# Optimization experiments

Hardware: AMD Instinct MI355X
Metric: run time of the kernel (lower is better)

## Reference

```python
import jax, jax.numpy as jnp
import numpy as np

N_NODES, SEQ, FEAT, HID, NLAYERS = 126, 24, 17, 100, 2


def setup_inputs() -> dict:
    key = jax.random.key(0)
    ks = jax.random.split(key, 14)
    B = 64
    s = 1.0 / np.sqrt(HID)  # torch LSTM default init scale
    inp = {
        "x": jax.random.normal(ks[0], (B, SEQ, N_NODES, FEAT), dtype=jnp.float32),
        # per-node stacked LSTM weights, gate order (i, f, g, o) as in torch
        "W_ih0": jax.random.uniform(ks[1], (N_NODES, 4 * HID, FEAT), jnp.float32, -s, s),
        "W_hh0": jax.random.uniform(ks[2], (N_NODES, 4 * HID, HID), jnp.float32, -s, s),
        "b_ih0": jax.random.uniform(ks[3], (N_NODES, 4 * HID), jnp.float32, -s, s),
        "b_hh0": jax.random.uniform(ks[4], (N_NODES, 4 * HID), jnp.float32, -s, s),
        "W_ih1": jax.random.uniform(ks[5], (N_NODES, 4 * HID, HID), jnp.float32, -s, s),
        "W_hh1": jax.random.uniform(ks[6], (N_NODES, 4 * HID, HID), jnp.float32, -s, s),
        "b_ih1": jax.random.uniform(ks[7], (N_NODES, 4 * HID), jnp.float32, -s, s),
        "b_hh1": jax.random.uniform(ks[8], (N_NODES, 4 * HID), jnp.float32, -s, s),
        "w_lin": jax.random.uniform(ks[9], (1, HID), jnp.float32, -s, s),
        "b_lin": jax.random.uniform(ks[10], (1,), jnp.float32, -s, s),
        "w_end": jax.random.uniform(ks[11], (1, SEQ), jnp.float32, -0.2, 0.2),  # Conv2d(seqlen->1, k=1)
        "b_end": jax.random.uniform(ks[12], (1,), jnp.float32, -0.2, 0.2),
    }
    return inp


def _lstm_cell(xin, h, c, Wih, Whh, bih, bhh):
    # xin: [N,B,Fin], h/c: [N,B,H], Wih: [N,4H,Fin], Whh: [N,4H,H]
    g = (jnp.einsum("nbf,ngf->nbg", xin, Wih)
         + jnp.einsum("nbh,ngh->nbg", h, Whh)
         + (bih + bhh)[:, None, :])
    i, f, gg, o = jnp.split(g, 4, axis=-1)
    c_new = jax.nn.sigmoid(f) * c + jax.nn.sigmoid(i) * jnp.tanh(gg)
    h_new = jax.nn.sigmoid(o) * jnp.tanh(c_new)
    return h_new, c_new


def reference(x, W_ih0, W_hh0, b_ih0, b_hh0, W_ih1, W_hh1, b_ih1, b_hh1,
              w_lin, b_lin, w_end, b_end):
    B, T, N, F = x.shape
    H = W_hh0.shape[-1]
    xt = jnp.transpose(x, (1, 2, 0, 3))  # [T, N, B, F]
    z = jnp.zeros((N, B, H), dtype=x.dtype)

    def step(carry, x_t):
        h1, c1, h2, c2 = carry
        h1, c1 = _lstm_cell(x_t, h1, c1, W_ih0, W_hh0, b_ih0, b_hh0)
        h2, c2 = _lstm_cell(h1, h2, c2, W_ih1, W_hh1, b_ih1, b_hh1)
        return (h1, c1, h2, c2), h2

    (h1, c1, h2, c2), outs = jax.lax.scan(step, (z, z, z, z), xt)  # outs: [T,N,B,H]
    lin = jnp.einsum("tnbh,oh->tnbo", outs, w_lin) + b_lin  # [T,N,B,1]
    lstmlayer = jnp.transpose(lin, (2, 0, 1, 3))  # [B,T,N,1] (matches torch permute(2,1,0,3))
    # Conv2d(seqlen -> out_channels=1, kernel 1x1) over the T channel axis
    out = jnp.einsum("btnj,ct->bcnj", lstmlayer, w_end) + b_end[None, :, None, None]  # [B,1,N,1]
    hn = jnp.stack([h1, h2], axis=1)  # [N, num_layers=2, B, H]
    cn = jnp.stack([c1, c2], axis=1)
    return (out, hn, cn)
```

## Files before the change

kernel.cpp:

```cpp
#include <hip/hip_runtime.h>
#include <hip/hip_bf16.h>

#define NN 126
#define TT 24
#define FF 17
#define HH 100
#define NMT 25

#define AL_SH 51200
#define X0_SH AL_SH
#define X1_SH (AL_SH + 8192)
#define X0BUF 4096
#define X1BUF 7168
#define TOT_SH (X1_SH + 2 * X1BUF)
#define LDS_BYTES (TOT_SH * 2)

typedef __attribute__((ext_vector_type(8))) short short8v;
typedef __attribute__((ext_vector_type(4))) float float4v;

__device__ __forceinline__ short f2bf(float f) {
    union { float f; unsigned u; } v; v.f = f;
    unsigned r = v.u + 0x7FFFu + ((v.u >> 16) & 1u);
    return (short)(r >> 16);
}
#define LOG2E 1.4426950408889634f
__device__ __forceinline__ float sigm_(float x) {
    return __builtin_amdgcn_rcpf(1.0f + __builtin_amdgcn_exp2f(-LOG2E * x));
}
__device__ __forceinline__ float tanh_(float x) {
    return 1.0f - 2.0f * __builtin_amdgcn_rcpf(1.0f + __builtin_amdgcn_exp2f((2.0f * LOG2E) * x));
}

__global__ __launch_bounds__(1024, 4)
void lstm_one(const float* __restrict__ x,
              const float* __restrict__ Wih0, const float* __restrict__ Whh0,
              const float* __restrict__ bih0, const float* __restrict__ bhh0,
              const float* __restrict__ Wih1, const float* __restrict__ Whh1,
              const float* __restrict__ bih1, const float* __restrict__ bhh1,
              const float* __restrict__ wlin, const float* __restrict__ blin,
              const float* __restrict__ wend, const float* __restrict__ bend,
              float* __restrict__ out)
{
    extern __shared__ short lds_s[];
    short* Al = lds_s;
    short* X0 = lds_s + X0_SH;
    short* X1 = lds_s + X1_SH;
    float* red = (float*)lds_s;

    const int n   = blockIdx.x >> 1;
    const int bh  = blockIdx.x & 1;
    const int tid = threadIdx.x, lane = tid & 63, w = tid >> 6;
    const int cl  = lane & 15, q = lane >> 4;
    const int mt0 = (w <= 8) ? (w * 2) : (18 + (w - 9));
    const int nmt = (w <= 8) ? 2 : 1;

    {
        const short8v zz = {0,0,0,0,0,0,0,0};
        for (int i = tid; i < TOT_SH / 8; i += 1024)
            *(short8v*)(lds_s + (size_t)i * 8) = zz;
    }
    __syncthreads();

    {
        const float* W = Whh0 + (size_t)n * 40000;
        for (int i = tid; i < 40000; i += 1024) {
            const int orl = i / 100, j = i - orl * 100;
            const int g = orl / 100, cell = orl - g * 100;
            const int gr = cell * 4 + g;
            const int k = 18 + j;
            Al[(((k >> 5) * NMT + (gr >> 4)) * 64 + ((((k >> 3) & 3) << 4) | (gr & 15))) * 8 + (k & 7)]
                = f2bf(W[i]);
        }
    }
    {
        const float* W = Wih0 + (size_t)n * 6800;
        for (int i = tid; i < 6800; i += 1024) {
            const int orl = i / 17, k = i - orl * 17;
            const int g = orl / 100, cell = orl - g * 100;
            const int gr = cell * 4 + g;
            Al[((gr >> 4) * 64 + ((((k >> 3) & 3) << 4) | (gr & 15))) * 8 + (k & 7)] = f2bf(W[i]);
        }
    }
    if (tid < 400) {
        const int g = tid / 100, cell = tid - g * 100;
        const int gr = cell * 4 + g;
        const int orow = n * 400 + tid;
        Al[((gr >> 4) * 64 + ((2 << 4) | (gr & 15))) * 8 + 1] = f2bf(bih0[orow] + bhh0[orow]);
    }

    short8v wreg[2][7];
    #pragma unroll
    for (int mi = 0; mi < 2; ++mi) {
        if (mi < nmt) {
            const int gr = (mt0 + mi) * 16 + cl;
            const int cell = gr >> 2, g = gr & 3;
            const int orow = n * 400 + g * HH + cell;
            const float* Wi = Wih1 + (size_t)orow * HH;
            const float* Wh = Whh1 + (size_t)orow * HH;
            #pragma unroll
            for (int kt = 0; kt < 7; ++kt) {
                const int k0 = kt * 32 + q * 8;
                float v[8];
                #pragma unroll
                for (int e = 0; e < 8; ++e) v[e] = 0.0f;
                if (k0 == 0) {
                    v[0] = bih1[orow] + bhh1[orow];
                    v[4] = Wi[0]; v[5] = Wi[1]; v[6] = Wi[2]; v[7] = Wi[3];
                } else if (k0 <= 96) {
                    #pragma unroll
                    for (int e = 0; e < 8; ++e) v[e] = Wi[k0 - 4 + e];
                } else if (k0 >= 104 && k0 <= 192) {
                    #pragma unroll
                    for (int e = 0; e < 8; ++e) v[e] = Wh[k0 - 104 + e];
                } else if (k0 == 200) {
                    v[0] = Wh[96]; v[1] = Wh[97]; v[2] = Wh[98]; v[3] = Wh[99];
                }
                short8v pv;
                #pragma unroll
                for (int e = 0; e < 8; ++e) pv[e] = f2bf(v[e]);
                wreg[mi][kt] = pv;
            }
        }
    }

    int aX0h1[2][2], aX1h1[2][2], aX1h2[2][2];
    #pragma unroll
    for (int mi = 0; mi < 2; ++mi) {
        const int cell = (mt0 + mi) * 4 + q;
        #pragma unroll
        for (int nh = 0; nh < 2; ++nh) {
            { const int k = 18 + cell;
              aX0h1[mi][nh] = (((k >> 5) * 2 + nh) * 64 + ((((k >> 3) & 3) << 4) | cl)) * 8 + (k & 7); }
            { const int k = 4 + cell;
              aX1h1[mi][nh] = (((k >> 5) * 2 + nh) * 64 + ((((k >> 3) & 3) << 4) | cl)) * 8 + (k & 7); }
            { const int k = 104 + cell;
              aX1h2[mi][nh] = (((k >> 5) * 2 + nh) * 64 + ((((k >> 3) & 3) << 4) | cl)) * 8 + (k & 7); }
        }
    }
    __syncthreads();

    if (tid < 32) X1[(((tid >> 4)) * 64 + (tid & 15)) * 8 + 0] = (short)0x3F80;
    if (w < 2) {
        const int b = bh * 32 + w * 16 + cl;
        const float* xr = x + ((size_t)b * TT + 0) * (NN * FF) + n * FF;
        if (q < 2) {
            short8v pv;
            #pragma unroll
            for (int e = 0; e < 8; ++e) pv[e] = f2bf(xr[q * 8 + e]);
            *(short8v*)(X0 + ((size_t)w * 64 + lane) * 8) = pv;
        } else if (q == 2) {
            const unsigned lo = (unsigned short)f2bf(xr[16]);
            *(unsigned*)(X0 + ((size_t)w * 64 + lane) * 8) = (0x3F80u << 16) | lo;
        }
    }
    __syncthreads();

    float c1[2][2], c2[2][2], macc[2][2];
    #pragma unroll
    for (int mi = 0; mi < 2; ++mi)
        #pragma unroll
        for (int nh = 0; nh < 2; ++nh) { c1[mi][nh] = 0.f; c2[mi][nh] = 0.f; macc[mi][nh] = 0.f; }

    for (int t = 0; t < TT; ++t) {
        const bool fin = (t == TT - 1);
        const int rb = t & 1;
        const int wb = rb ^ 1;
        float4v acc[2][2];

        #pragma unroll
        for (int mi = 0; mi < 2; ++mi) { acc[mi][0] = (float4v){0,0,0,0}; acc[mi][1] = (float4v){0,0,0,0}; }
        {
            const short* X0r = X0 + rb * X0BUF;
            #pragma unroll
            for (int kt = 0; kt < 4; ++kt) {
                const short8v b0 = *(const short8v*)(X0r + (((size_t)kt * 2 + 0) * 64 + lane) * 8);
                const short8v b1 = *(const short8v*)(X0r + (((size_t)kt * 2 + 1) * 64 + lane) * 8);
                #pragma unroll
                for (int mi = 0; mi < 2; ++mi) {
                    if (mi < nmt) {
                        const short8v a = *(const short8v*)(
                            Al + (((size_t)kt * NMT + (mt0 + mi)) * 64 + lane) * 8);
                        acc[mi][0] = __builtin_amdgcn_mfma_f32_16x16x32_bf16(a, b0, acc[mi][0], 0, 0, 0);
                        acc[mi][1] = __builtin_amdgcn_mfma_f32_16x16x32_bf16(a, b1, acc[mi][1], 0, 0, 0);
                    }
                }
            }
        }
        #pragma unroll
        for (int mi = 0; mi < 2; ++mi) {
            if (mi < nmt) {
                const int cell = (mt0 + mi) * 4 + q;
                #pragma unroll
                for (int nh = 0; nh < 2; ++nh) {
                    const float iv = sigm_(acc[mi][nh][0]);
                    const float fv = sigm_(acc[mi][nh][1]);
                    const float gv = tanh_(acc[mi][nh][2]);
                    const float ov = sigm_(acc[mi][nh][3]);
                    const float c  = fv * c1[mi][nh] + iv * gv;
                    c1[mi][nh] = c;
                    const float h = ov * tanh_(c);
                    const short hb = f2bf(h);
                    X0[wb * X0BUF + aX0h1[mi][nh]] = hb;
                    X1[aX1h1[mi][nh]] = hb;
                    if (fin) {
                        const int b = bh * 32 + nh * 16 + cl;
                        out[8064 + ((size_t)(n * 2 + 0) * 64 + b) * HH + cell] = h;
                        out[8064 + 1612800 + ((size_t)(n * 2 + 0) * 64 + b) * HH + cell] = c;
                    }
                }
            }
        }
        __syncthreads();

        float xv0 = 0.f, xv1 = 0.f, xv2 = 0.f, xv3 = 0.f, xv4 = 0.f, xv5 = 0.f, xv6 = 0.f, xv7 = 0.f;
        const bool doX = (w < 2) && (t + 1 < TT);
        if (doX) {
            const int b = bh * 32 + w * 16 + cl;
            const float* xr = x + ((size_t)b * TT + (t + 1)) * (NN * FF) + n * FF;
            if (q < 2) {
                const int k0 = q * 8;
                xv0 = xr[k0 + 0]; xv1 = xr[k0 + 1]; xv2 = xr[k0 + 2]; xv3 = xr[k0 + 3];
                xv4 = xr[k0 + 4]; xv5 = xr[k0 + 5]; xv6 = xr[k0 + 6]; xv7 = xr[k0 + 7];
            } else if (q == 2) {
                xv0 = xr[16];
            }
        }

        #pragma unroll
        for (int mi = 0; mi < 2; ++mi) { acc[mi][0] = (float4v){0,0,0,0}; acc[mi][1] = (float4v){0,0,0,0}; }
        {
            const short* X1h2 = X1 + rb * X1BUF;
            const int kt3sel = (q == 0) ? 0 : rb * X1BUF;
            #pragma unroll
            for (int kt = 0; kt < 7; ++kt) {
                const short* base = (kt < 3) ? X1 : ((kt == 3) ? (X1 + kt3sel) : X1h2);
                const short8v b0 = *(const short8v*)(base + (((size_t)kt * 2 + 0) * 64 + lane) * 8);
                const short8v b1 = *(const short8v*)(base + (((size_t)kt * 2 + 1) * 64 + lane) * 8);
                #pragma unroll
                for (int mi = 0; mi < 2; ++mi) {
                    if (mi < nmt) {
                        acc[mi][0] = __builtin_amdgcn_mfma_f32_16x16x32_bf16(wreg[mi][kt], b0, acc[mi][0], 0, 0, 0);
                        acc[mi][1] = __builtin_amdgcn_mfma_f32_16x16x32_bf16(wreg[mi][kt], b1, acc[mi][1], 0, 0, 0);
                    }
                }
            }
        }
        const float wet = wend[t];
        #pragma unroll
        for (int mi = 0; mi < 2; ++mi) {
            if (mi < nmt) {
                const int cell = (mt0 + mi) * 4 + q;
                #pragma unroll
                for (int nh = 0; nh < 2; ++nh) {
                    const float iv = sigm_(acc[mi][nh][0]);
                    const float fv = sigm_(acc[mi][nh][1]);
                    const float gv = tanh_(acc[mi][nh][2]);
                    const float ov = sigm_(acc[mi][nh][3]);
                    const float c  = fv * c2[mi][nh] + iv * gv;
                    c2[mi][nh] = c;
                    const float h = ov * tanh_(c);
                    macc[mi][nh] = fmaf(wet, h, macc[mi][nh]);
                    if (!fin) X1[wb * X1BUF + aX1h2[mi][nh]] = f2bf(h);
                    if (fin) {
                        const int b = bh * 32 + nh * 16 + cl;
                        out[8064 + ((size_t)(n * 2 + 1) * 64 + b) * HH + cell] = h;
                        out[8064 + 1612800 + ((size_t)(n * 2 + 1) * 64 + b) * HH + cell] = c;
                    }
                }
            }
        }
        if (doX) {
            short* X0w = X0 + wb * X0BUF;
            if (q < 2) {
                short8v pv;
                pv[0] = f2bf(xv0); pv[1] = f2bf(xv1); pv[2] = f2bf(xv2); pv[3] = f2bf(xv3);
                pv[4] = f2bf(xv4); pv[5] = f2bf(xv5); pv[6] = f2bf(xv6); pv[7] = f2bf(xv7);
                *(short8v*)(X0w + ((size_t)w * 64 + lane) * 8) = pv;
            } else if (q == 2) {
                const unsigned lo = (unsigned short)f2bf(xv0);
                *(unsigned*)(X0w + ((size_t)w * 64 + lane) * 8) = (0x3F80u << 16) | lo;
            }
        }
        __syncthreads();
    }

    #pragma unroll
    for (int mi = 0; mi < 2; ++mi) {
        if (mi < nmt) {
            const int cell = (mt0 + mi) * 4 + q;
            #pragma unroll
            for (int nh = 0; nh < 2; ++nh)
                red[cell * 32 + nh * 16 + cl] = wlin[cell] * macc[mi][nh];
        }
    }
    __syncthreads();
    if (tid < 32) {
        float s = 0.0f;
        for (int j = 0; j < HH; ++j) s += red[j * 32 + tid];
        float ws = 0.0f;
        for (int t2 = 0; t2 < TT; ++t2) ws += wend[t2];
        s += blin[0] * ws + bend[0];
        out[(size_t)(bh * 32 + tid) * NN + n] = s;
    }
}

extern "C" void kernel_launch(void* const* d_in, const int* in_sizes, int n_in,
                              void* d_out, int out_size, void* d_ws, size_t ws_size,
                              hipStream_t stream) {
    const float* x    = (const float*)d_in[0];
    const float* Wih0 = (const float*)d_in[1];
    const float* Whh0 = (const float*)d_in[2];
    const float* bih0 = (const float*)d_in[3];
    const float* bhh0 = (const float*)d_in[4];
    const float* Wih1 = (const float*)d_in[5];
    const float* Whh1 = (const float*)d_in[6];
    const float* bih1 = (const float*)d_in[7];
    const float* bhh1 = (const float*)d_in[8];
    const float* wlin = (const float*)d_in[9];
    const float* blin = (const float*)d_in[10];
    const float* wend = (const float*)d_in[11];
    const float* bend = (const float*)d_in[12];
    (void)d_ws; (void)ws_size; (void)in_sizes; (void)n_in; (void)out_size;

    lstm_one<<<dim3(NN * 2), dim3(1024), LDS_BYTES, stream>>>(
        x, Wih0, Whh0, bih0, bhh0, Wih1, Whh1, bih1, bhh1,
        wlin, blin, wend, bend, (float*)d_out);
}
```

Before: 111.9 us.

## Skew LSTM layers so layer-1 and layer-2 steps share one barrier

Restructures the time loop into a wavefront schedule: iteration i computes layer 1 at step i and layer 2 at step i-1. Layer-2's input h1 is now double-buffered in X1, so both layers run between a single __syncthreads per iteration instead of two. This halves the barrier count and lets layer-1 and layer-2 work overlap, at the cost of one extra loop iteration and an extra buffer for the bias/h1 region.

```diff
diff --git a/kernel.cpp b/kernel.cpp
--- a/kernel.cpp
+++ b/kernel.cpp
@@ -32,14 +32,14 @@
 }
 
 __global__ __launch_bounds__(1024, 4)
-void lstm_one(const float* __restrict__ x,
-              const float* __restrict__ Wih0, const float* __restrict__ Whh0,
-              const float* __restrict__ bih0, const float* __restrict__ bhh0,
-              const float* __restrict__ Wih1, const float* __restrict__ Whh1,
-              const float* __restrict__ bih1, const float* __restrict__ bhh1,
-              const float* __restrict__ wlin, const float* __restrict__ blin,
-              const float* __restrict__ wend, const float* __restrict__ bend,
-              float* __restrict__ out)
+void lstm_skew(const float* __restrict__ x,
+               const float* __restrict__ Wih0, const float* __restrict__ Whh0,
+               const float* __restrict__ bih0, const float* __restrict__ bhh0,
+               const float* __restrict__ Wih1, const float* __restrict__ Whh1,
+               const float* __restrict__ bih1, const float* __restrict__ bhh1,
+               const float* __restrict__ wlin, const float* __restrict__ blin,
+               const float* __restrict__ wend, const float* __restrict__ bend,
+               float* __restrict__ out)
 {
     extern __shared__ short lds_s[];
     short* Al = lds_s;
@@ -139,7 +139,11 @@
     }
     __syncthreads();
 
-    if (tid < 32) X1[(((tid >> 4)) * 64 + (tid & 15)) * 8 + 0] = (short)0x3F80;
+    if (tid < 32) {
+        const int off = (((tid >> 4)) * 64 + (tid & 15)) * 8 + 0;
+        X1[off] = (short)0x3F80;
+        X1[X1BUF + off] = (short)0x3F80;
+    }
     if (w < 2) {
         const int b = bh * 32 + w * 16 + cl;
         const float* xr = x + ((size_t)b * TT + 0) * (NN * FF) + n * FF;
@@ -161,124 +165,126 @@
         #pragma unroll
         for (int nh = 0; nh < 2; ++nh) { c1[mi][nh] = 0.f; c2[mi][nh] = 0.f; macc[mi][nh] = 0.f; }
 
-    for (int t = 0; t < TT; ++t) {
-        const bool fin = (t == TT - 1);
-        const int rb = t & 1;
+    for (int i = 0; i <= TT; ++i) {
+        const int rb = i & 1;
         const int wb = rb ^ 1;
         float4v acc[2][2];
 
-        #pragma unroll
-        for (int mi = 0; mi < 2; ++mi) { acc[mi][0] = (float4v){0,0,0,0}; acc[mi][1] = (float4v){0,0,0,0}; }
-        {
-            const short* X0r = X0 + rb * X0BUF;
-            #pragma unroll
-            for (int kt = 0; kt < 4; ++kt) {
-                const short8v b0 = *(const short8v*)(X0r + (((size_t)kt * 2 + 0) * 64 + lane) * 8);
-                const short8v b1 = *(const short8v*)(X0r + (((size_t)kt * 2 + 1) * 64 + lane) * 8);
+        if (i < TT) {
+            float xv0 = 0.f, xv1 = 0.f, xv2 = 0.f, xv3 = 0.f, xv4 = 0.f, xv5 = 0.f, xv6 = 0.f, xv7 = 0.f;
+            const bool doX = (w < 2) && (i + 1 < TT);
+            if (doX) {
+                const int b = bh * 32 + w * 16 + cl;
+                const float* xr = x + ((size_t)b * TT + (i + 1)) * (NN * FF) + n * FF;
+                if (q < 2) {
+                    const int k0 = q * 8;
+                    xv0 = xr[k0 + 0]; xv1 = xr[k0 + 1]; xv2 = xr[k0 + 2]; xv3 = xr[k0 + 3];
+                    xv4 = xr[k0 + 4]; xv5 = xr[k0 + 5]; xv6 = xr[k0 + 6]; xv7 = xr[k0 + 7];
+                } else if (q == 2) {
+                    xv0 = xr[16];
+                }
+            }
+
+            #pragma unroll
+            for (int mi = 0; mi < 2; ++mi) { acc[mi][0] = (float4v){0,0,0,0}; acc[mi][1] = (float4v){0,0,0,0}; }
+            {
+                const short* X0r = X0 + rb * X0BUF;
                 #pragma unroll
-                for (int mi = 0; mi < 2; ++mi) {
-                    if (mi < nmt) {
-                        const short8v a = *(const short8v*)(
-                            Al + (((size_t)kt * NMT + (mt0 + mi)) * 64 + lane) * 8);
-                        acc[mi][0] = __builtin_amdgcn_mfma_f32_16x16x32_bf16(a, b0, acc[mi][0], 0, 0, 0);
-                        acc[mi][1] = __builtin_amdgcn_mfma_f32_16x16x32_bf16(a, b1, acc[mi][1], 0, 0, 0);
+                for (int kt = 0; kt < 4; ++kt) {
+                    const short8v b0 = *(const short8v*)(X0r + (((size_t)kt * 2 + 0) * 64 + lane) * 8);
+                    const short8v b1 = *(const short8v*)(X0r + (((size_t)kt * 2 + 1) * 64 + lane) * 8);
+                    #pragma unroll
+                    for (int mi = 0; mi < 2; ++mi) {
+                        if (mi < nmt) {
+                            const short8v a = *(const short8v*)(
+                                Al + (((size_t)kt * NMT + (mt0 + mi)) * 64 + lane) * 8);
+                            acc[mi][0] = __builtin_amdgcn_mfma_f32_16x16x32_bf16(a, b0, acc[mi][0], 0, 0, 0);
+                            acc[mi][1] = __builtin_amdgcn_mfma_f32_16x16x32_bf16(a, b1, acc[mi][1], 0, 0, 0);
+                        }
                     }
                 }
             }
-        }
-        #pragma unroll
-        for (int mi = 0; mi < 2; ++mi) {
-            if (mi < nmt) {
-                const int cell = (mt0 + mi) * 4 + q;
+            const bool fin0 = (i == TT - 1);
+            #pragma unroll
+            for (int mi = 0; mi < 2; ++mi) {
+                if (mi < nmt) {
+                    const int cell = (mt0 + mi) * 4 + q;
+                    #pragma unroll
+                    for (int nh = 0; nh < 2; ++nh) {
+                        const float iv = sigm_(acc[mi][nh][0]);
+                        const float fv = sigm_(acc[mi][nh][1]);
+                        const float gv = tanh_(acc[mi][nh][2]);
+                        const float ov = sigm_(acc[mi][nh][3]);
+                        const float c  = fv * c1[mi][nh] + iv * gv;
+                        c1[mi][nh] = c;
+                        const float h = ov * tanh_(c);
+                        const short hb = f2bf(h);
+                        X0[wb * X0BUF + aX0h1[mi][nh]] = hb;
+                        X1[wb * X1BUF + aX1h1[mi][nh]] = hb;
+                        if (fin0) {
+                            const int b = bh * 32 + nh * 16 + cl;
+                            out[8064 + ((size_t)(n * 2 + 0) * 64 + b) * HH + cell] = h;
+                            out[8064 + 1612800 + ((size_t)(n * 2 + 0) * 64 + b) * HH + cell] = c;
+                        }
+                    }
+                }
+            }
+            if (doX) {
+                short* X0w = X0 + wb * X0BUF;
+                if (q < 2) {
+                    short8v pv;
+                    pv[0] = f2bf(xv0); pv[1] = f2bf(xv1); pv[2] = f2bf(xv2); pv[3] = f2bf(xv3);
+                    pv[4] = f2bf(xv4); pv[5] = f2bf(xv5); pv[6] = f2bf(xv6); pv[7] = f2bf(xv7);
+                    *(short8v*)(X0w + ((size_t)w * 64 + lane) * 8) = pv;
+                } else if (q == 2) {
+                    const unsigned lo = (unsigned short)f2bf(xv0);
+                    *(unsigned*)(X0w + ((size_t)w * 64 + lane) * 8) = (0x3F80u << 16) | lo;
+                }
+            }
+        }
+
+        if (i > 0) {
+            #pragma unroll
+            for (int mi = 0; mi < 2; ++mi) { acc[mi][0] = (float4v){0,0,0,0}; acc[mi][1] = (float4v){0,0,0,0}; }
+            {
+                const short* X1r = X1 + rb * X1BUF;
                 #pragma unroll
-                for (int nh = 0; nh < 2; ++nh) {
-                    const float iv = sigm_(acc[mi][nh][0]);
-                    const float fv = sigm_(acc[mi][nh][1]);
-                    const float gv = tanh_(acc[mi][nh][2]);
-                    const float ov = sigm_(acc[mi][nh][3]);
-                    const float c  = fv * c1[mi][nh] + iv * gv;
-                    c1[mi][nh] = c;
-                    const float h = ov * tanh_(c);
-                    const short hb = f2bf(h);
-                    X0[wb * X0BUF + aX0h1[mi][nh]] = hb;
-                    X1[aX1h1[mi][nh]] = hb;
-                    if (fin) {
-                        const int b = bh * 32 + nh * 16 + cl;
-                        out[8064 + ((size_t)(n * 2 + 0) * 64 + b) * HH + cell] = h;
-                        out[8064 + 1612800 + ((size_t)(n * 2 + 0) * 64 + b) * HH + cell] = c;
+                for (int kt = 0; kt < 7; ++kt) {
+                    const short8v b0 = *(const short8v*)(X1r + (((size_t)kt * 2 + 0) * 64 + lane) * 8);
+                    const short8v b1 = *(const short8v*)(X1r + (((size_t)kt * 2 + 1) * 64 + lane) * 8);
+                    #pragma unroll
+                    for (int mi = 0; mi < 2; ++mi) {
+                        if (mi < nmt) {
+                            acc[mi][0] = __builtin_amdgcn_mfma_f32_16x16x32_bf16(wreg[mi][kt], b0, acc[mi][0], 0, 0, 0);
+                            acc[mi][1] = __builtin_amdgcn_mfma_f32_16x16x32_bf16(wreg[mi][kt], b1, acc[mi][1], 0, 0, 0);
+                        }
                     }
                 }
             }
-        }
-        __syncthreads();
-
-        float xv0 = 0.f, xv1 = 0.f, xv2 = 0.f, xv3 = 0.f, xv4 = 0.f, xv5 = 0.f, xv6 = 0.f, xv7 = 0.f;
-        const bool doX = (w < 2) && (t + 1 < TT);
-        if (doX) {
-            const int b = bh * 32 + w * 16 + cl;
-            const float* xr = x + ((size_t)b * TT + (t + 1)) * (NN * FF) + n * FF;
-            if (q < 2) {
-                const int k0 = q * 8;
-                xv0 = xr[k0 + 0]; xv1 = xr[k0 + 1]; xv2 = xr[k0 + 2]; xv3 = xr[k0 + 3];
-                xv4 = xr[k0 + 4]; xv5 = xr[k0 + 5]; xv6 = xr[k0 + 6]; xv7 = xr[k0 + 7];
-            } else if (q == 2) {
-                xv0 = xr[16];
-            }
-        }
-
-        #pragma unroll
-        for (int mi = 0; mi < 2; ++mi) { acc[mi][0] = (float4v){0,0,0,0}; acc[mi][1] = (float4v){0,0,0,0}; }
-        {
-            const short* X1h2 = X1 + rb * X1BUF;
-            const int kt3sel = (q == 0) ? 0 : rb * X1BUF;
-            #pragma unroll
-            for (int kt = 0; kt < 7; ++kt) {
-                const short* base = (kt < 3) ? X1 : ((kt == 3) ? (X1 + kt3sel) : X1h2);
-                const short8v b0 = *(const short8v*)(base + (((size_t)kt * 2 + 0) * 64 + lane) * 8);
-                const short8v b1 = *(const short8v*)(base + (((size_t)kt * 2 + 1) * 64 + lane) * 8);
-                #pragma unroll
-                for (int mi = 0; mi < 2; ++mi) {
-                    if (mi < nmt) {
-                        acc[mi][0] = __builtin_amdgcn_mfma_f32_16x16x32_bf16(wreg[mi][kt], b0, acc[mi][0], 0, 0, 0);
-                        acc[mi][1] = __builtin_amdgcn_mfma_f32_16x16x32_bf16(wreg[mi][kt], b1, acc[mi][1], 0, 0, 0);
+            const float wet = wend[i - 1];
+            const bool fin1 = (i == TT);
+            #pragma unroll
+            for (int mi = 0; mi < 2; ++mi) {
+                if (mi < nmt) {
+                    const int cell = (mt0 + mi) * 4 + q;
+                    #pragma unroll
+                    for (int nh = 0; nh < 2; ++nh) {
+                        const float iv = sigm_(acc[mi][nh][0]);
+                        const float fv = sigm_(acc[mi][nh][1]);
+                        const float gv = tanh_(acc[mi][nh][2]);
+                        const float ov = sigm_(acc[mi][nh][3]);
+                        const float c  = fv * c2[mi][nh] + iv * gv;
+                        c2[mi][nh] = c;
+                        const float h = ov * tanh_(c);
+                        macc[mi][nh] = fmaf(wet, h, macc[mi][nh]);
+                        if (!fin1) X1[wb * X1BUF + aX1h2[mi][nh]] = f2bf(h);
+                        if (fin1) {
+                            const int b = bh * 32 + nh * 16 + cl;
+                            out[8064 + ((size_t)(n * 2 + 1) * 64 + b) * HH + cell] = h;
+                            out[8064 + 1612800 + ((size_t)(n * 2 + 1) * 64 + b) * HH + cell] = c;
+                        }
                     }
                 }
-            }
-        }
-        const float wet = wend[t];
-        #pragma unroll
-        for (int mi = 0; mi < 2; ++mi) {
-            if (mi < nmt) {
-                const int cell = (mt0 + mi) * 4 + q;
-                #pragma unroll
-                for (int nh = 0; nh < 2; ++nh) {
-                    const float iv = sigm_(acc[mi][nh][0]);
-                    const float fv = sigm_(acc[mi][nh][1]);
-                    const float gv = tanh_(acc[mi][nh][2]);
-                    const float ov = sigm_(acc[mi][nh][3]);
-                    const float c  = fv * c2[mi][nh] + iv * gv;
-                    c2[mi][nh] = c;
-                    const float h = ov * tanh_(c);
-                    macc[mi][nh] = fmaf(wet, h, macc[mi][nh]);
-                    if (!fin) X1[wb * X1BUF + aX1h2[mi][nh]] = f2bf(h);
-                    if (fin) {
-                        const int b = bh * 32 + nh * 16 + cl;
-                        out[8064 + ((size_t)(n * 2 + 1) * 64 + b) * HH + cell] = h;
-                        out[8064 + 1612800 + ((size_t)(n * 2 + 1) * 64 + b) * HH + cell] = c;
-                    }
-                }
-            }
-        }
-        if (doX) {
-            short* X0w = X0 + wb * X0BUF;
-            if (q < 2) {
-                short8v pv;
-                pv[0] = f2bf(xv0); pv[1] = f2bf(xv1); pv[2] = f2bf(xv2); pv[3] = f2bf(xv3);
-                pv[4] = f2bf(xv4); pv[5] = f2bf(xv5); pv[6] = f2bf(xv6); pv[7] = f2bf(xv7);
-                *(short8v*)(X0w + ((size_t)w * 64 + lane) * 8) = pv;
-            } else if (q == 2) {
-                const unsigned lo = (unsigned short)f2bf(xv0);
-                *(unsigned*)(X0w + ((size_t)w * 64 + lane) * 8) = (0x3F80u << 16) | lo;
             }
         }
         __syncthreads();
@@ -322,7 +328,7 @@
     const float* bend = (const float*)d_in[12];
     (void)d_ws; (void)ws_size; (void)in_sizes; (void)n_in; (void)out_size;
 
-    lstm_one<<<dim3(NN * 2), dim3(1024), LDS_BYTES, stream>>>(
+    lstm_skew<<<dim3(NN * 2), dim3(1024), LDS_BYTES, stream>>>(
         x, Wih0, Whh0, bih0, bhh0, Wih1, Whh1, bih1, bhh1,
         wlin, blin, wend, bend, (float*)d_out);
 }
```

Measured after the change: 116.1 us. +3.8%, slower.
